# Kernel tuning notes

Hardware: AMD Instinct MI355X
Metric: run time of the kernel (lower is better)

The kernel has to match this reference:

```python
import jax, jax.numpy as jnp
import numpy as np

B, L, D = 1, 2048, 2048
H, KV, HD = 32, 8, 64
REP = H // KV  # GQA repeat factor = 4


def _rope(t, cos, sin):
    # t: (B, L, nH, HD); cos/sin: (L, HD//2). Complex rotation on (even, odd) pairs.
    tr = t.reshape(*t.shape[:-1], HD // 2, 2)
    xr, xi = tr[..., 0], tr[..., 1]
    c = cos[None, :, None, :]
    s = sin[None, :, None, :]
    out_r = xr * c - xi * s
    out_i = xr * s + xi * c
    return jnp.stack([out_r, out_i], axis=-1).reshape(t.shape)


def setup_inputs() -> dict:
    key = jax.random.key(0)
    ks = jax.random.split(key, 5)
    x = jax.random.normal(ks[0], (B, L, D), jnp.float32)
    wq = jax.random.normal(ks[1], (D, H * HD), jnp.float32) * 0.02
    wk = jax.random.normal(ks[2], (D, KV * HD), jnp.float32) * 0.02
    wv = jax.random.normal(ks[3], (D, KV * HD), jnp.float32) * 0.02
    wo = jax.random.normal(ks[4], (H * HD, D), jnp.float32) * 0.02
    pos = jnp.arange(L, dtype=jnp.float32)
    inv_freq = 1.0 / (10000.0 ** (jnp.arange(0, HD, 2, dtype=jnp.float32) / HD))
    ang = pos[:, None] * inv_freq[None, :]  # (L, HD//2)
    freqs_cos = jnp.cos(ang)
    freqs_sin = jnp.sin(ang)
    # causal additive mask (L, L): 0 on/below diagonal, large negative above
    causal = jnp.arange(L)[None, :] <= jnp.arange(L)[:, None]
    mask = jnp.where(causal, 0.0, -1e9).astype(jnp.float32)
    return {"x": x, "wq": wq, "wk": wk, "wv": wv, "wo": wo,
            "freqs_cos": freqs_cos, "freqs_sin": freqs_sin, "mask": mask}


def reference(x, wq, wk, wv, wo, freqs_cos, freqs_sin, mask):
    q = (x @ wq).reshape(B, L, H, HD)
    k = (x @ wk).reshape(B, L, KV, HD)
    v = (x @ wv).reshape(B, L, KV, HD)
    q = _rope(q, freqs_cos, freqs_sin)
    k = _rope(k, freqs_cos, freqs_sin)
    # GQA: repeat_interleave kv heads
    k = jnp.repeat(k, REP, axis=2)
    v = jnp.repeat(v, REP, axis=2)
    # (B, nH, L, HD)
    q = q.transpose(0, 2, 1, 3)
    k = k.transpose(0, 2, 1, 3)
    v = v.transpose(0, 2, 1, 3)
    scores = jnp.einsum('bhqd,bhkd->bhqk', q, k) / np.float32(np.sqrt(HD))
    scores = scores + mask[None, None, :, :]
    attn = jax.nn.softmax(scores.astype(jnp.float32), axis=-1).astype(q.dtype)
    out = jnp.einsum('bhqk,bhkd->bqhd', attn, v).reshape(B, L, H * HD)
    return out @ wo
```

## Files before the change

### kernel.cpp

```cpp
#include <hip/hip_runtime.h>
#include <hip/hip_bf16.h>

#define L 2048
#define D 2048
#define NH 32
#define NKV 8
#define HD 64

typedef unsigned short u16;
typedef __attribute__((ext_vector_type(8))) short bf16x8;
typedef __attribute__((ext_vector_type(4))) float f32x4;

#define QSCALE 0.1803368801f

__device__ __forceinline__ u16 f2bf(float x) {
    __hip_bfloat16 b = __float2bfloat16(x);
    return *reinterpret_cast<u16*>(&b);
}

__device__ __forceinline__ void gload_lds16(const void* g, void* l) {
    __builtin_amdgcn_global_load_lds(
        (const __attribute__((address_space(1))) unsigned int*)g,
        (__attribute__((address_space(3))) unsigned int*)l, 16, 0, 0);
}

__global__ __launch_bounds__(256) void prep_kernel(
    const float* __restrict__ x, u16* __restrict__ xb,
    const float* __restrict__ wq, const float* __restrict__ wk,
    const float* __restrict__ wv, const float* __restrict__ wo,
    u16* __restrict__ wqkvT, u16* __restrict__ woT)
{
    const int z = blockIdx.z;
    if (z == 4) {
        int i = (blockIdx.y * 64 + blockIdx.x) * 256 + threadIdx.x;
        float4 v = ((const float4*)x)[i];
        ushort4 o;
        o.x = f2bf(v.x); o.y = f2bf(v.y); o.z = f2bf(v.z); o.w = f2bf(v.w);
        ((ushort4*)xb)[i] = o;
        return;
    }
    const float* src; u16* dst; int C;
    if (z == 0)      { src = wq; dst = wqkvT;                           C = 2048; }
    else if (z == 1) { src = wk; dst = wqkvT + (size_t)2048 * 2048;     C = 512;  }
    else if (z == 2) { src = wv; dst = wqkvT + (size_t)2560 * 2048;     C = 512;  }
    else             { src = wo; dst = woT;                             C = 2048; }
    const int c0 = blockIdx.x * 32;
    if (c0 >= C) return;
    const int r0 = blockIdx.y * 32;
    __shared__ float tile[32][33];
    const int tx = threadIdx.x & 31, ty = threadIdx.x >> 5;
#pragma unroll
    for (int i = 0; i < 32; i += 8)
        tile[ty + i][tx] = src[(size_t)(r0 + ty + i) * C + c0 + tx];
    __syncthreads();
#pragma unroll
    for (int i = 0; i < 32; i += 8)
        dst[(size_t)(c0 + ty + i) * 2048 + r0 + tx] = f2bf(tile[tx][ty + i]);
}

#define VT_LDS 72

template <int MODE>
__global__ __launch_bounds__(256) void gemm4w_kernel(
    const u16* __restrict__ A, const u16* __restrict__ Bt, void* __restrict__ Cout,
    int N, int K, const float* __restrict__ fc, const float* __restrict__ fs,
    u16* __restrict__ vt)
{
    __shared__ __align__(16) u16 As[4][128 * 32];
    __shared__ __align__(16) u16 Bs[4][128 * 32];
    const int tid = threadIdx.x;
    const int w = tid >> 6, lane = tid & 63;

    const int nwg = (int)(gridDim.x * gridDim.y);
    int bid = (int)blockIdx.y * (int)gridDim.x + (int)blockIdx.x;
    bid = (bid & 7) * (nwg >> 3) + (bid >> 3);
    const int m0 = (bid / (int)gridDim.x) * 128, n0 = (bid % (int)gridDim.x) * 128;

    const int l15 = lane & 15, quad = lane >> 4, q8 = quad * 8;
    const int sr = lane >> 2, sc = (lane & 3) * 8;
    const int wr = (w >> 1) * 64, wc = (w & 1) * 64;

    const u16* pa0 = A  + (size_t)(m0 + w * 16 + sr) * K + sc;
    const u16* pa1 = A  + (size_t)(m0 + 64 + w * 16 + sr) * K + sc;
    const u16* pb0 = Bt + (size_t)(n0 + w * 16 + sr) * K + sc;
    const u16* pb1 = Bt + (size_t)(n0 + 64 + w * 16 + sr) * K + sc;

    f32x4 acc[4][4];
#pragma unroll
    for (int i = 0; i < 4; ++i)
#pragma unroll
        for (int j = 0; j < 4; ++j) acc[i][j] = (f32x4){0.f, 0.f, 0.f, 0.f};

    const int nSub = K / 32;
    const int nOut = nSub / 2;
#pragma unroll
    for (int s = 0; s < 4; ++s) {
        const int ko = s * 32;
        gload_lds16(pa0 + ko, &As[s][(w * 16) * 32]);
        gload_lds16(pa1 + ko, &As[s][(64 + w * 16) * 32]);
        gload_lds16(pb0 + ko, &Bs[s][(w * 16) * 32]);
        gload_lds16(pb1 + ko, &Bs[s][(64 + w * 16) * 32]);
    }
    for (int it = 0; it < nOut; ++it) {
        const int s0 = 2 * it, cb0 = s0 & 3, cb1 = (s0 + 1) & 3;
        asm volatile("s_waitcnt vmcnt(8)" ::: "memory");
        asm volatile("s_barrier" ::: "memory");
        bf16x8 a0[4], a1[4], b0[4], b1[4];
#pragma unroll
        for (int t = 0; t < 4; ++t) {
            a0[t] = *(const bf16x8*)&As[cb0][(wr + t * 16 + l15) * 32 + q8];
            b0[t] = *(const bf16x8*)&Bs[cb0][(wc + t * 16 + l15) * 32 + q8];
            a1[t] = *(const bf16x8*)&As[cb1][(wr + t * 16 + l15) * 32 + q8];
            b1[t] = *(const bf16x8*)&Bs[cb1][(wc + t * 16 + l15) * 32 + q8];
        }
        asm volatile("s_waitcnt lgkmcnt(0)" ::: "memory");
        asm volatile("s_barrier" ::: "memory");
        {
            const int sp0 = s0 + 4, sp1 = s0 + 5;
            const int k0 = (sp0 < nSub) ? sp0 * 32 : 0;
            const int k1 = (sp1 < nSub) ? sp1 * 32 : 0;
            gload_lds16(pa0 + k0, &As[cb0][(w * 16) * 32]);
            gload_lds16(pa1 + k0, &As[cb0][(64 + w * 16) * 32]);
            gload_lds16(pb0 + k0, &Bs[cb0][(w * 16) * 32]);
            gload_lds16(pb1 + k0, &Bs[cb0][(64 + w * 16) * 32]);
            gload_lds16(pa0 + k1, &As[cb1][(w * 16) * 32]);
            gload_lds16(pa1 + k1, &As[cb1][(64 + w * 16) * 32]);
            gload_lds16(pb0 + k1, &Bs[cb1][(w * 16) * 32]);
            gload_lds16(pb1 + k1, &Bs[cb1][(64 + w * 16) * 32]);
        }
#pragma unroll
        for (int i = 0; i < 4; ++i)
#pragma unroll
            for (int j = 0; j < 4; ++j) {
                acc[i][j] = __builtin_amdgcn_mfma_f32_16x16x32_bf16(a0[i], b0[j], acc[i][j], 0, 0, 0);
                acc[i][j] = __builtin_amdgcn_mfma_f32_16x16x32_bf16(a1[i], b1[j], acc[i][j], 0, 0, 0);
            }
    }

    if (MODE == 0) {
        float* C = (float*)Cout;
#pragma unroll
        for (int i = 0; i < 4; ++i)
#pragma unroll
            for (int j = 0; j < 4; ++j)
#pragma unroll
                for (int r = 0; r < 4; ++r)
                    C[(size_t)(m0 + wr + i * 16 + quad * 4 + r) * N + n0 + wc + j * 16 + l15] = acc[i][j][r];
    } else {
        __syncthreads();
        u16* O = (u16*)Cout;
        const int vc0 = n0 + wc;
        if (vc0 < 2560) {
            const float scl = (vc0 < 2048) ? QSCALE : 1.0f;
            const int odd = l15 & 1;
#pragma unroll
            for (int i = 0; i < 4; ++i)
#pragma unroll
                for (int j = 0; j < 4; ++j)
#pragma unroll
                    for (int r = 0; r < 4; ++r) {
                        const int row = m0 + wr + i * 16 + quad * 4 + r;
                        const int col = vc0 + j * 16 + l15;
                        float v = acc[i][j][r];
                        const int i2 = (j * 16 + l15) >> 1;
                        const float c = fc[row * 32 + i2], s = fs[row * 32 + i2];
                        const float p = __shfl_xor(v, 1);
                        float o = (odd ? (p * s + v * c) : (v * c - p * s)) * scl;
                        O[(size_t)row * 3072 + col] = f2bf(o);
                    }
        } else {
            u16* ws_ = (w < 2 ? (u16*)As : (u16*)Bs) + (w & 1) * (64 * VT_LDS);
#pragma unroll
            for (int i = 0; i < 4; ++i)
#pragma unroll
                for (int j = 0; j < 4; ++j)
#pragma unroll
                    for (int r = 0; r < 4; ++r)
                        ws_[(j * 16 + l15) * VT_LDS + i * 16 + quad * 4 + r] = f2bf(acc[i][j][r]);
#pragma unroll
            for (int t = 0; t < 8; ++t) {
                const int vr = t * 8 + (lane >> 3);
                const int c8 = (lane & 7) * 8;
                bf16x8 vv = *(const bf16x8*)&ws_[vr * VT_LDS + c8];
                *(bf16x8*)&vt[(size_t)(vc0 - 2560 + vr) * 2048 + m0 + wr + c8] = vv;
            }
        }
    }
}

#define ATT_LDK 72
#define ATT_LDP 72

__global__ __launch_bounds__(256) void attn_mfma_kernel(
    const u16* __restrict__ qkv,
    const u16* __restrict__ vt,
    u16* __restrict__ ob)
{
    __shared__ __align__(16) u16 Ks[64 * ATT_LDK];
    __shared__ __align__(16) u16 Vs[64 * ATT_LDK];
    __shared__ __align__(16) u16 Ps[4][16 * ATT_LDP];

    const int h = blockIdx.x;
    const int tile = (int)gridDim.y - 1 - (int)blockIdx.y;
    const int gkv = h >> 2;
    const int tid = threadIdx.x;
    const int w = tid >> 6, lane = tid & 63;
    const int l15 = lane & 15, quad = lane >> 4;
    const int q0 = tile * 64 + w * 16;

    bf16x8 ones;
#pragma unroll
    for (int j = 0; j < 8; ++j) ones[j] = (short)0x3F80;

    bf16x8 qa[2];
    {
        const u16* qrow = qkv + (size_t)(q0 + l15) * 3072 + h * HD + quad * 8;
        qa[0] = *(const bf16x8*)(qrow);
        qa[1] = *(const bf16x8*)(qrow + 32);
    }
    f32x4 O[4];
#pragma unroll
    for (int i = 0; i < 4; ++i) O[i] = (f32x4){0.f, 0.f, 0.f, 0.f};
    float m_run[4], l_run[4];
#pragma unroll
    for (int r = 0; r < 4; ++r) { m_run[r] = -1e30f; l_run[r] = 0.f; }

    const int sslot = tid, sr0 = sslot >> 3, so8 = (sslot & 7) * 8;
    const int sslot1 = tid + 256, sr1 = sslot1 >> 3, so81 = (sslot1 & 7) * 8;

    uint4 kreg[2], vreg[2];
    kreg[0] = *(const uint4*)&qkv[(size_t)(sr0) * 3072 + 2048 + gkv * HD + so8];
    vreg[0] = *(const uint4*)&vt[(size_t)(gkv * HD + sr0) * 2048 + so8];
    kreg[1] = *(const uint4*)&qkv[(size_t)(sr1) * 3072 + 2048 + gkv * HD + so81];
    vreg[1] = *(const uint4*)&vt[(size_t)(gkv * HD + sr1) * 2048 + so81];

    for (int c = 0; c <= tile; ++c) {
        __syncthreads();
        *(uint4*)&Ks[sr0 * ATT_LDK + so8]  = kreg[0];
        *(uint4*)&Vs[sr0 * ATT_LDK + so8]  = vreg[0];
        *(uint4*)&Ks[sr1 * ATT_LDK + so81] = kreg[1];
        *(uint4*)&Vs[sr1 * ATT_LDK + so81] = vreg[1];
        __syncthreads();
        if (c < tile) {
            const int kn = (c + 1) * 64;
            kreg[0] = *(const uint4*)&qkv[(size_t)(kn + sr0) * 3072 + 2048 + gkv * HD + so8];
            vreg[0] = *(const uint4*)&vt[(size_t)(gkv * HD + sr0) * 2048 + kn + so8];
            kreg[1] = *(const uint4*)&qkv[(size_t)(kn + sr1) * 3072 + 2048 + gkv * HD + so81];
            vreg[1] = *(const uint4*)&vt[(size_t)(gkv * HD + sr1) * 2048 + kn + so81];
        }

        f32x4 S[4];
        __builtin_amdgcn_s_setprio(1);
#pragma unroll
        for (int kt = 0; kt < 4; ++kt) {
            bf16x8 b0 = *(const bf16x8*)&Ks[(kt * 16 + l15) * ATT_LDK + quad * 8];
            bf16x8 b1 = *(const bf16x8*)&Ks[(kt * 16 + l15) * ATT_LDK + 32 + quad * 8];
            f32x4 s = (f32x4){0.f, 0.f, 0.f, 0.f};
            s = __builtin_amdgcn_mfma_f32_16x16x32_bf16(qa[0], b0, s, 0, 0, 0);
            s = __builtin_amdgcn_mfma_f32_16x16x32_bf16(qa[1], b1, s, 0, 0, 0);
            S[kt] = s;
        }
        __builtin_amdgcn_s_setprio(0);
        if (c == tile) {
#pragma unroll
            for (int kt = 0; kt < 4; ++kt) {
                int keyl = kt * 16 + l15;
#pragma unroll
                for (int r = 0; r < 4; ++r)
                    if (keyl > w * 16 + quad * 4 + r) S[kt][r] = -1e30f;
            }
        }
        float alpha[4];
#pragma unroll
        for (int r = 0; r < 4; ++r) {
            float mx = fmaxf(fmaxf(S[0][r], S[1][r]), fmaxf(S[2][r], S[3][r]));
#pragma unroll
            for (int off = 1; off < 16; off <<= 1) mx = fmaxf(mx, __shfl_xor(mx, off));
            float mn = fmaxf(m_run[r], mx);
            alpha[r] = exp2f(m_run[r] - mn);
            m_run[r] = mn;
#pragma unroll
            for (int kt = 0; kt < 4; ++kt) S[kt][r] = exp2f(S[kt][r] - mn);
        }
        u16* pw = Ps[w];
#pragma unroll
        for (int kt = 0; kt < 4; ++kt)
#pragma unroll
            for (int r = 0; r < 4; ++r)
                pw[(quad * 4 + r) * ATT_LDP + kt * 16 + l15] = f2bf(S[kt][r]);
        bf16x8 pa0 = *(const bf16x8*)&pw[l15 * ATT_LDP + quad * 8];
        bf16x8 pa1 = *(const bf16x8*)&pw[l15 * ATT_LDP + 32 + quad * 8];

        f32x4 rs = (f32x4){0.f, 0.f, 0.f, 0.f};
        rs = __builtin_amdgcn_mfma_f32_16x16x32_bf16(pa0, ones, rs, 0, 0, 0);
        rs = __builtin_amdgcn_mfma_f32_16x16x32_bf16(pa1, ones, rs, 0, 0, 0);
#pragma unroll
        for (int r = 0; r < 4; ++r) l_run[r] = l_run[r] * alpha[r] + rs[r];

#pragma unroll
        for (int dt = 0; dt < 4; ++dt)
#pragma unroll
            for (int r = 0; r < 4; ++r) O[dt][r] *= alpha[r];
        __builtin_amdgcn_s_setprio(1);
#pragma unroll
        for (int dt = 0; dt < 4; ++dt) {
            bf16x8 b0 = *(const bf16x8*)&Vs[(dt * 16 + l15) * ATT_LDK + quad * 8];
            bf16x8 b1 = *(const bf16x8*)&Vs[(dt * 16 + l15) * ATT_LDK + 32 + quad * 8];
            O[dt] = __builtin_amdgcn_mfma_f32_16x16x32_bf16(pa0, b0, O[dt], 0, 0, 0);
            O[dt] = __builtin_amdgcn_mfma_f32_16x16x32_bf16(pa1, b1, O[dt], 0, 0, 0);
        }
        __builtin_amdgcn_s_setprio(0);
    }
#pragma unroll
    for (int r = 0; r < 4; ++r) {
        float inv = 1.0f / l_run[r];
        u16* orow = ob + (size_t)(q0 + quad * 4 + r) * 2048 + h * HD;
#pragma unroll
        for (int dt = 0; dt < 4; ++dt)
            orow[dt * 16 + l15] = f2bf(O[dt][r] * inv);
    }
}

extern "C" void kernel_launch(void* const* d_in, const int* in_sizes, int n_in,
                              void* d_out, int out_size, void* d_ws, size_t ws_size,
                              hipStream_t stream)
{
    const float* x  = (const float*)d_in[0];
    const float* wq = (const float*)d_in[1];
    const float* wk = (const float*)d_in[2];
    const float* wv = (const float*)d_in[3];
    const float* wo = (const float*)d_in[4];
    const float* fc = (const float*)d_in[5];
    const float* fs = (const float*)d_in[6];
    float* out = (float*)d_out;

    u16* xb     = (u16*)d_ws;
    u16* wqkvT  = xb     + (size_t)2048 * 2048;
    u16* woT    = wqkvT  + (size_t)3072 * 2048;
    u16* qkv_bf = woT    + (size_t)2048 * 2048;
    u16* vt     = qkv_bf + (size_t)2048 * 3072;
    u16* ab     = vt     + (size_t)512 * 2048;

    prep_kernel<<<dim3(64, 64, 5), 256, 0, stream>>>(x, xb, wq, wk, wv, wo, wqkvT, woT);

    gemm4w_kernel<1><<<dim3(3072 / 128, 2048 / 128), 256, 0, stream>>>(
        xb, wqkvT, qkv_bf, 3072, 2048, fc, fs, vt);

    attn_mfma_kernel<<<dim3(NH, L / 64), 256, 0, stream>>>(qkv_bf, vt, ab);

    gemm4w_kernel<0><<<dim3(2048 / 128, 2048 / 128), 256, 0, stream>>>(
        ab, woT, out, 2048, 2048, nullptr, nullptr, nullptr);
}
```

Baseline: 299.9 us.

## Store GEMM operands in pre-tiled panel layout for contiguous LDS loads

```diff
diff --git a/kernel.cpp b/kernel.cpp
--- a/kernel.cpp
+++ b/kernel.cpp
@@ -12,6 +12,8 @@
 typedef __attribute__((ext_vector_type(4))) float f32x4;
 
 #define QSCALE 0.1803368801f
+
+#define PANEL_OFF(d0, k) ((((size_t)((d0) >> 7) * 64 + ((k) >> 5)) << 12) + (((d0) & 127) << 5) + ((k) & 31))
 
 __device__ __forceinline__ u16 f2bf(float x) {
     __hip_bfloat16 b = __float2bfloat16(x);
@@ -33,10 +35,12 @@
     const int z = blockIdx.z;
     if (z == 4) {
         int i = (blockIdx.y * 64 + blockIdx.x) * 256 + threadIdx.x;
+        int e = i * 4;
+        int row = e >> 11, k0 = e & 2047;
         float4 v = ((const float4*)x)[i];
         ushort4 o;
         o.x = f2bf(v.x); o.y = f2bf(v.y); o.z = f2bf(v.z); o.w = f2bf(v.w);
-        ((ushort4*)xb)[i] = o;
+        *(ushort4*)&xb[PANEL_OFF(row, k0)] = o;
         return;
     }
     const float* src; u16* dst; int C;
@@ -54,8 +58,10 @@
         tile[ty + i][tx] = src[(size_t)(r0 + ty + i) * C + c0 + tx];
     __syncthreads();
 #pragma unroll
-    for (int i = 0; i < 32; i += 8)
-        dst[(size_t)(c0 + ty + i) * 2048 + r0 + tx] = f2bf(tile[tx][ty + i]);
+    for (int i = 0; i < 32; i += 8) {
+        const int n = c0 + ty + i, k = r0 + tx;
+        dst[PANEL_OFF(n, k)] = f2bf(tile[tx][ty + i]);
+    }
 }
 
 #define VT_LDS 72
@@ -77,13 +83,12 @@
     const int m0 = (bid / (int)gridDim.x) * 128, n0 = (bid % (int)gridDim.x) * 128;
 
     const int l15 = lane & 15, quad = lane >> 4, q8 = quad * 8;
-    const int sr = lane >> 2, sc = (lane & 3) * 8;
     const int wr = (w >> 1) * 64, wc = (w & 1) * 64;
-
-    const u16* pa0 = A  + (size_t)(m0 + w * 16 + sr) * K + sc;
-    const u16* pa1 = A  + (size_t)(m0 + 64 + w * 16 + sr) * K + sc;
-    const u16* pb0 = Bt + (size_t)(n0 + w * 16 + sr) * K + sc;
-    const u16* pb1 = Bt + (size_t)(n0 + 64 + w * 16 + sr) * K + sc;
+    const int l8 = lane * 8;
+    const int wch = w * 1024;
+
+    const u16* pa = A  + ((size_t)(m0 >> 7) * (K / 32) << 12);
+    const u16* pb = Bt + ((size_t)(n0 >> 7) * (K / 32) << 12);
 
     f32x4 acc[4][4];
 #pragma unroll
@@ -95,11 +100,11 @@
     const int nOut = nSub / 2;
 #pragma unroll
     for (int s = 0; s < 4; ++s) {
-        const int ko = s * 32;
-        gload_lds16(pa0 + ko, &As[s][(w * 16) * 32]);
-        gload_lds16(pa1 + ko, &As[s][(64 + w * 16) * 32]);
-        gload_lds16(pb0 + ko, &Bs[s][(w * 16) * 32]);
-        gload_lds16(pb1 + ko, &Bs[s][(64 + w * 16) * 32]);
+        const size_t so = (size_t)s << 12;
+        gload_lds16(pa + so + wch + l8,       &As[s][wch]);
+        gload_lds16(pa + so + wch + 512 + l8, &As[s][wch + 512]);
+        gload_lds16(pb + so + wch + l8,       &Bs[s][wch]);
+        gload_lds16(pb + so + wch + 512 + l8, &Bs[s][wch + 512]);
     }
     for (int it = 0; it < nOut; ++it) {
         const int s0 = 2 * it, cb0 = s0 & 3, cb1 = (s0 + 1) & 3;
@@ -117,16 +122,16 @@
         asm volatile("s_barrier" ::: "memory");
         {
             const int sp0 = s0 + 4, sp1 = s0 + 5;
-            const int k0 = (sp0 < nSub) ? sp0 * 32 : 0;
-            const int k1 = (sp1 < nSub) ? sp1 * 32 : 0;
-            gload_lds16(pa0 + k0, &As[cb0][(w * 16) * 32]);
-            gload_lds16(pa1 + k0, &As[cb0][(64 + w * 16) * 32]);
-            gload_lds16(pb0 + k0, &Bs[cb0][(w * 16) * 32]);
-            gload_lds16(pb1 + k0, &Bs[cb0][(64 + w * 16) * 32]);
-            gload_lds16(pa0 + k1, &As[cb1][(w * 16) * 32]);
-            gload_lds16(pa1 + k1, &As[cb1][(64 + w * 16) * 32]);
-            gload_lds16(pb0 + k1, &Bs[cb1][(w * 16) * 32]);
-            gload_lds16(pb1 + k1, &Bs[cb1][(64 + w * 16) * 32]);
+            const size_t k0 = (size_t)((sp0 < nSub) ? sp0 : 0) << 12;
+            const size_t k1 = (size_t)((sp1 < nSub) ? sp1 : 0) << 12;
+            gload_lds16(pa + k0 + wch + l8,       &As[cb0][wch]);
+            gload_lds16(pa + k0 + wch + 512 + l8, &As[cb0][wch + 512]);
+            gload_lds16(pb + k0 + wch + l8,       &Bs[cb0][wch]);
+            gload_lds16(pb + k0 + wch + 512 + l8, &Bs[cb0][wch + 512]);
+            gload_lds16(pa + k1 + wch + l8,       &As[cb1][wch]);
+            gload_lds16(pa + k1 + wch + 512 + l8, &As[cb1][wch + 512]);
+            gload_lds16(pb + k1 + wch + l8,       &Bs[cb1][wch]);
+            gload_lds16(pb + k1 + wch + 512 + l8, &Bs[cb1][wch + 512]);
         }
 #pragma unroll
         for (int i = 0; i < 4; ++i)
@@ -194,7 +199,7 @@
 __global__ __launch_bounds__(256) void attn_mfma_kernel(
     const u16* __restrict__ qkv,
     const u16* __restrict__ vt,
-    u16* __restrict__ ob)
+    u16* __restrict__ ab)
 {
     __shared__ __align__(16) u16 Ks[64 * ATT_LDK];
     __shared__ __align__(16) u16 Vs[64 * ATT_LDK];
@@ -225,32 +230,21 @@
 #pragma unroll
     for (int r = 0; r < 4; ++r) { m_run[r] = -1e30f; l_run[r] = 0.f; }
 
-    const int sslot = tid, sr0 = sslot >> 3, so8 = (sslot & 7) * 8;
-    const int sslot1 = tid + 256, sr1 = sslot1 >> 3, so81 = (sslot1 & 7) * 8;
-
-    uint4 kreg[2], vreg[2];
-    kreg[0] = *(const uint4*)&qkv[(size_t)(sr0) * 3072 + 2048 + gkv * HD + so8];
-    vreg[0] = *(const uint4*)&vt[(size_t)(gkv * HD + sr0) * 2048 + so8];
-    kreg[1] = *(const uint4*)&qkv[(size_t)(sr1) * 3072 + 2048 + gkv * HD + so81];
-    vreg[1] = *(const uint4*)&vt[(size_t)(gkv * HD + sr1) * 2048 + so81];
-
     for (int c = 0; c <= tile; ++c) {
+        const int key0 = c * 64;
         __syncthreads();
-        *(uint4*)&Ks[sr0 * ATT_LDK + so8]  = kreg[0];
-        *(uint4*)&Vs[sr0 * ATT_LDK + so8]  = vreg[0];
-        *(uint4*)&Ks[sr1 * ATT_LDK + so81] = kreg[1];
-        *(uint4*)&Vs[sr1 * ATT_LDK + so81] = vreg[1];
+#pragma unroll
+        for (int i = 0; i < 2; ++i) {
+            int slot = tid + 256 * i;
+            int r = slot >> 3, o8 = (slot & 7) * 8;
+            *(uint4*)&Ks[r * ATT_LDK + o8] =
+                *(const uint4*)&qkv[(size_t)(key0 + r) * 3072 + 2048 + gkv * HD + o8];
+            *(uint4*)&Vs[r * ATT_LDK + o8] =
+                *(const uint4*)&vt[(size_t)(gkv * HD + r) * 2048 + key0 + o8];
+        }
         __syncthreads();
-        if (c < tile) {
-            const int kn = (c + 1) * 64;
-            kreg[0] = *(const uint4*)&qkv[(size_t)(kn + sr0) * 3072 + 2048 + gkv * HD + so8];
-            vreg[0] = *(const uint4*)&vt[(size_t)(gkv * HD + sr0) * 2048 + kn + so8];
-            kreg[1] = *(const uint4*)&qkv[(size_t)(kn + sr1) * 3072 + 2048 + gkv * HD + so81];
-            vreg[1] = *(const uint4*)&vt[(size_t)(gkv * HD + sr1) * 2048 + kn + so81];
-        }
 
         f32x4 S[4];
-        __builtin_amdgcn_s_setprio(1);
 #pragma unroll
         for (int kt = 0; kt < 4; ++kt) {
             bf16x8 b0 = *(const bf16x8*)&Ks[(kt * 16 + l15) * ATT_LDK + quad * 8];
@@ -260,7 +254,6 @@
             s = __builtin_amdgcn_mfma_f32_16x16x32_bf16(qa[1], b1, s, 0, 0, 0);
             S[kt] = s;
         }
-        __builtin_amdgcn_s_setprio(0);
         if (c == tile) {
 #pragma unroll
             for (int kt = 0; kt < 4; ++kt) {
@@ -301,7 +294,6 @@
         for (int dt = 0; dt < 4; ++dt)
 #pragma unroll
             for (int r = 0; r < 4; ++r) O[dt][r] *= alpha[r];
-        __builtin_amdgcn_s_setprio(1);
 #pragma unroll
         for (int dt = 0; dt < 4; ++dt) {
             bf16x8 b0 = *(const bf16x8*)&Vs[(dt * 16 + l15) * ATT_LDK + quad * 8];
@@ -309,15 +301,16 @@
             O[dt] = __builtin_amdgcn_mfma_f32_16x16x32_bf16(pa0, b0, O[dt], 0, 0, 0);
             O[dt] = __builtin_amdgcn_mfma_f32_16x16x32_bf16(pa1, b1, O[dt], 0, 0, 0);
         }
-        __builtin_amdgcn_s_setprio(0);
     }
 #pragma unroll
     for (int r = 0; r < 4; ++r) {
         float inv = 1.0f / l_run[r];
-        u16* orow = ob + (size_t)(q0 + quad * 4 + r) * 2048 + h * HD;
-#pragma unroll
-        for (int dt = 0; dt < 4; ++dt)
-            orow[dt * 16 + l15] = f2bf(O[dt][r] * inv);
+        const int q = q0 + quad * 4 + r;
+#pragma unroll
+        for (int dt = 0; dt < 4; ++dt) {
+            const int col = h * HD + dt * 16 + l15;
+            ab[PANEL_OFF(q, col)] = f2bf(O[dt][r] * inv);
+        }
     }
 }
 
```

Result: faster. 278.0 us (-7.3%).
